# Kernel optimization log

Hardware: AMD Instinct MI355X
Metric: run time of the kernel (lower is better)

## Reference

```python
import jax, jax.numpy as jnp
import numpy as np

C0 = 32   # number of 0e (scalar) channels
C1 = 16   # number of 1o (vector) channels
NG = 1024 # num_graphs
N = 300000
F = C0 * (C0 + 1) // 2 + C1 * (C1 + 1) // 2  # 664 invariant outputs of TensorSquare->0e


def setup_inputs() -> dict:
    key = jax.random.key(0)
    k1, k2, k3 = jax.random.split(key, 3)
    node_ft = jax.random.normal(k1, (N, C0 + 3 * C1), dtype=jnp.float32)
    batch_index = jnp.sort(jax.random.randint(k2, (N,), 0, NG, dtype=jnp.int32))
    # o3.Linear-style init: normal / sqrt(fan_in)
    W = jax.random.normal(k3, (F, 1), dtype=jnp.float32) / np.float32(np.sqrt(F))
    return {"node_ft": node_ft, "batch_index": batch_index, "num_graphs": NG, "W": W}


def tensor_square_0e(node_ft):
    # Equivariant tensor square keeping only 0e (invariant) outputs:
    #  - symmetric products of scalar channels s_i * s_j (i<=j)
    #  - dot products of vector channels v_i . v_j (i<=j), component-normalized
    s = node_ft[:, :C0]                      # [N, C0]
    v = node_ft[:, C0:].reshape(-1, C1, 3)   # [N, C1, 3]
    i0, j0 = jnp.triu_indices(C0)
    i1, j1 = jnp.triu_indices(C1)
    ts_s = s[:, i0] * s[:, j0]                                  # [N, 528]
    vdot = jnp.einsum('nic,njc->nij', v, v) / jnp.float32(np.sqrt(3.0))
    ts_v = vdot[:, i1, j1]                                      # [N, 136]
    return jnp.concatenate([ts_s, ts_v], axis=1)                # [N, 664]


def reference(node_ft, batch_index, num_graphs, W):
    x = tensor_square_0e(node_ft)            # [N, F]
    x = jax.nn.selu(x)
    x = x @ W                                # [N, 1] attention logits (1x0e)
    ex = jnp.exp(x)                          # [N, 1]
    z = jax.ops.segment_sum(ex, batch_index, num_segments=num_graphs)  # [G, 1]
    attn = ex / z[batch_index]               # segment softmax weights [N, 1]
    out = jax.ops.segment_sum(node_ft * attn, batch_index, num_segments=num_graphs)
    return out                               # [G, C0 + 3*C1]
```

## Files before the change

kernel.cpp:

```cpp
#include <hip/hip_runtime.h>


typedef float f2 __attribute__((ext_vector_type(2)));

#define C0 32
#define C1 16
#define NODE_F 80
#define NG_CONST 1024
#define NPB 128
#define TPB 256
#define NCHUNK 6

#define SELU_SCALE 1.0507009873554804934193349852946
#define SELU_ALPHA 1.6732632423543772848170429916717
#define LOG2E      1.4426950408889634073599246810019

#define CS_SCALE 1.2011224087864498f
#define CV_SCALE 0.91271231102878545f

#define WS_S 0
#define WS_Z 81920
#define WS_W 82944

__device__ __forceinline__ int ks_idx(int i, int j) { return i * C0 - (i * (i - 1)) / 2 + (j - i); }
__device__ __forceinline__ int kv_idx(int i, int j) { return 528 + i * C1 - (i * (i - 1)) / 2 + (j - i); }

__global__ __launch_bounds__(256) void prep_kernel(
    const float* __restrict__ W, float* __restrict__ ws)
{
    const int t = blockIdx.x * blockDim.x + threadIdx.x;
    if (t < 82944) {
        ws[t] = 0.0f;
    } else {
        int u = t - 82944;
        if (u < 512) {
            int i = u >> 4, q = u & 15;
            int j0 = 2 * q, j1 = 2 * q + 1;
            ws[WS_W + 2 * u]     = (j0 >= i) ? W[ks_idx(i, j0)] : 0.0f;
            ws[WS_W + 2 * u + 1] = (j1 >= i) ? W[ks_idx(i, j1)] : 0.0f;
        } else if (u < 640) {
            int v = u - 512;
            int i = v >> 3, q = v & 7;
            int j0 = 2 * q, j1 = 2 * q + 1;
            ws[WS_W + 1024 + 2 * v]     = (j0 >= i) ? W[kv_idx(i, j0)] : 0.0f;
            ws[WS_W + 1024 + 2 * v + 1] = (j1 >= i) ? W[kv_idx(i, j1)] : 0.0f;
        }
    }
}

__global__ __launch_bounds__(TPB, 4) void main_kernel(
    const float* __restrict__ nf, const int* __restrict__ bi,
    const float* __restrict__ ws, float* __restrict__ S,
    float* __restrict__ z, int N)
{
    __shared__ __align__(16) float Wlds[1280];
    __shared__ float exl[NPB];
    __shared__ int   bil[NPB];

    const int tid  = threadIdx.x;
    const int base = blockIdx.x * NPB;
    const float4* g4 = (const float4*)nf;

    #pragma unroll
    for (int u = tid; u < 1280; u += TPB) Wlds[u] = ws[WS_W + u];

    if (tid < NPB) {
        int idx = base + tid;
        bil[tid] = bi[idx > N - 1 ? N - 1 : idx];
    }

    const int  ln    = tid >> 1;
    const int  p     = tid & 1;
    const int  n     = base + ln;
    const bool valid = (n < N);
    const int  nn    = valid ? n : (N - 1);
    __syncthreads();

    const float4* gp = g4 + (size_t)nn * 20;
    const f2* WsL = (const f2*)Wlds;
    const f2* WvL = (const f2*)(Wlds + 1024);

    f2 s2[C0 / 2];
    {
        float4 rs[8];
        #pragma unroll
        for (int q = 0; q < 8; ++q) rs[q] = gp[q];
        #pragma unroll
        for (int q = 0; q < 8; ++q) {
            s2[2 * q]     = f2{rs[q].x, rs[q].y} * CS_SCALE;
            s2[2 * q + 1] = f2{rs[q].z, rs[q].w} * CS_SCALE;
        }
    }
    #pragma unroll
    for (int q = 0; q < C0 / 2; ++q) asm volatile("" : "+v"(s2[q]));

    f2 accA[2], accB[2];
    accA[0] = (f2)0.f; accA[1] = (f2)0.f; accB[0] = (f2)0.f; accB[1] = (f2)0.f;

    #pragma unroll
    for (int k = 0; k < C0 / 2; ++k) {
        const int i = 2 * k + p;
        const float si = p ? s2[k].y : s2[k].x;
        const f2 si2 = f2{si, si};
        #pragma unroll
        for (int q = k; q < C0 / 2; ++q) {
            f2 f = si2 * s2[q];
            f2 pp = __builtin_elementwise_max(f, (f2)0.f);
            f2 m  = __builtin_elementwise_min(f, (f2)0.f);
            f2 e; e.x = __builtin_amdgcn_exp2f(m.x);
                  e.y = __builtin_amdgcn_exp2f(m.y);
            f2 w = WsL[i * 16 + q];
            accA[q & 1] = __builtin_elementwise_fma(w, pp, accA[q & 1]);
            accB[q & 1] = __builtin_elementwise_fma(w, e, accB[q & 1]);
        }
    }

    float4 rv[12];
    #pragma unroll
    for (int q = 0; q < 12; ++q) rv[q] = gp[8 + q];

    f2 vp[C1 / 2][3];
    {
        const float* rvf = (const float*)rv;
        #pragma unroll
        for (int q = 0; q < C1 / 2; ++q) {
            #pragma unroll
            for (int c = 0; c < 3; ++c)
                vp[q][c] = f2{rvf[6 * q + c], rvf[6 * q + 3 + c]} * CV_SCALE;
        }
    }

    #pragma unroll
    for (int k = 0; k < C1 / 2; ++k) {
        const int i = 2 * k + p;
        const float vi0 = p ? vp[k][0].y : vp[k][0].x;
        const float vi1 = p ? vp[k][1].y : vp[k][1].x;
        const float vi2 = p ? vp[k][2].y : vp[k][2].x;
        #pragma unroll
        for (int q = k; q < C1 / 2; ++q) {
            f2 f = vp[q][0] * f2{vi0, vi0};
            f = __builtin_elementwise_fma(vp[q][1], f2{vi1, vi1}, f);
            f = __builtin_elementwise_fma(vp[q][2], f2{vi2, vi2}, f);
            f2 pp = __builtin_elementwise_max(f, (f2)0.f);
            f2 m  = __builtin_elementwise_min(f, (f2)0.f);
            f2 e; e.x = __builtin_amdgcn_exp2f(m.x);
                  e.y = __builtin_amdgcn_exp2f(m.y);
            f2 w = WvL[i * 8 + q];
            accA[q & 1] = __builtin_elementwise_fma(w, pp, accA[q & 1]);
            accB[q & 1] = __builtin_elementwise_fma(w, e, accB[q & 1]);
        }
    }

    float A1 = accA[0].x + accA[0].y + accA[1].x + accA[1].y;
    float A2 = accB[0].x + accB[0].y + accB[1].x + accB[1].y;
    A1 += __shfl_xor(A1, 1);
    A2 += __shfl_xor(A2, 1);
    const float l2 = fmaf((float)SELU_SCALE, A1,
                          (float)(SELU_SCALE * SELU_ALPHA * LOG2E) * A2);
    if (p == 0) exl[ln] = valid ? __builtin_amdgcn_exp2f(l2) : 0.0f;
    __syncthreads();

    if (tid < NCHUNK * 20) {
        const int no = tid / 20;
        const int c4 = tid % 20;
        const int nb = (no * NPB) / NCHUNK;
        const int ne = ((no + 1) * NPB) / NCHUNK;
        int cg = bil[nb];
        float4 acc = make_float4(0.f, 0.f, 0.f, 0.f);
        float  zacc = 0.0f;

        for (int nl = nb; nl < ne; ++nl) {
            const int g2 = bil[nl];
            if (g2 != cg) {
                unsafeAtomicAdd(&S[cg * NODE_F + c4 * 4 + 0], acc.x);
                unsafeAtomicAdd(&S[cg * NODE_F + c4 * 4 + 1], acc.y);
                unsafeAtomicAdd(&S[cg * NODE_F + c4 * 4 + 2], acc.z);
                unsafeAtomicAdd(&S[cg * NODE_F + c4 * 4 + 3], acc.w);
                if (c4 == 0) unsafeAtomicAdd(&z[cg], zacc);
                acc = make_float4(0.f, 0.f, 0.f, 0.f); zacc = 0.0f; cg = g2;
            }
            int idx = base + nl; if (idx > N - 1) idx = N - 1;
            const float  w = exl[nl];
            const float4 v = g4[(size_t)idx * 20 + c4];
            acc.x = fmaf(v.x, w, acc.x); acc.y = fmaf(v.y, w, acc.y);
            acc.z = fmaf(v.z, w, acc.z); acc.w = fmaf(v.w, w, acc.w);
            zacc += w;
        }
        unsafeAtomicAdd(&S[cg * NODE_F + c4 * 4 + 0], acc.x);
        unsafeAtomicAdd(&S[cg * NODE_F + c4 * 4 + 1], acc.y);
        unsafeAtomicAdd(&S[cg * NODE_F + c4 * 4 + 2], acc.z);
        unsafeAtomicAdd(&S[cg * NODE_F + c4 * 4 + 3], acc.w);
        if (c4 == 0) unsafeAtomicAdd(&z[cg], zacc);
    }
}

__global__ __launch_bounds__(256) void divide_kernel(
    const float* __restrict__ S, const float* __restrict__ z,
    float* __restrict__ out)
{
    const int t = blockIdx.x * blockDim.x + threadIdx.x;
    if (t >= NG_CONST * NODE_F) return;
    const float zz = z[t / NODE_F];
    out[t] = (zz > 0.0f) ? (S[t] / zz) : 0.0f;
}

extern "C" void kernel_launch(void* const* d_in, const int* in_sizes, int n_in,
                              void* d_out, int out_size, void* d_ws, size_t ws_size,
                              hipStream_t stream) {
    const float* nf = (const float*)d_in[0];
    const int*   bi = (const int*)d_in[1];
    const float* W  = (const float*)d_in[3];
    float* out = (float*)d_out;

    const int N = in_sizes[0] / NODE_F;
    float* ws = (float*)d_ws;
    float* S  = ws + WS_S;
    float* z  = ws + WS_Z;

    hipLaunchKernelGGL(prep_kernel, dim3(332), dim3(256), 0, stream, W, ws);
    hipLaunchKernelGGL(main_kernel, dim3((N + NPB - 1) / NPB), dim3(TPB), 0, stream,
                       nf, bi, ws, S, z, N);
    hipLaunchKernelGGL(divide_kernel, dim3((NG_CONST * NODE_F + 255) / 256), dim3(256),
                       0, stream, S, z, out);
}
```

Measured before the change: 182.3 us.

## Split each node's tensor-square across four threads with padded LDS weight rows

Each node's pairwise product work is now split across four threads instead of two, and the block size doubles to 512 threads for the same 128 nodes. The weight table in LDS is repacked with padded row strides of 17 and 9, likely to avoid bank conflicts when four lanes read different rows. The aim is more parallelism per node and shorter per-thread dependency chains. The cost is an extra shuffle stage and redundant node loads in four threads, and the launch-bounds minimum-blocks hint of 4 at 512 threads may tighten the register budget.

After: 187.9 us. +3.1%, slower.

```diff
diff --git a/kernel.cpp b/kernel.cpp
--- a/kernel.cpp
+++ b/kernel.cpp
@@ -8,7 +8,7 @@
 #define NODE_F 80
 #define NG_CONST 1024
 #define NPB 128
-#define TPB 256
+#define TPB 512
 #define NCHUNK 6
 
 #define SELU_SCALE 1.0507009873554804934193349852946
@@ -33,17 +33,25 @@
         ws[t] = 0.0f;
     } else {
         int u = t - 82944;
-        if (u < 512) {
-            int i = u >> 4, q = u & 15;
-            int j0 = 2 * q, j1 = 2 * q + 1;
-            ws[WS_W + 2 * u]     = (j0 >= i) ? W[ks_idx(i, j0)] : 0.0f;
-            ws[WS_W + 2 * u + 1] = (j1 >= i) ? W[ks_idx(i, j1)] : 0.0f;
-        } else if (u < 640) {
-            int v = u - 512;
-            int i = v >> 3, q = v & 7;
-            int j0 = 2 * q, j1 = 2 * q + 1;
-            ws[WS_W + 1024 + 2 * v]     = (j0 >= i) ? W[kv_idx(i, j0)] : 0.0f;
-            ws[WS_W + 1024 + 2 * v + 1] = (j1 >= i) ? W[kv_idx(i, j1)] : 0.0f;
+        if (u < 1088) {
+            int fu = u >> 1, comp = u & 1;
+            int i = fu / 17, q = fu % 17;
+            float val = 0.0f;
+            if (q < 16) {
+                int j = 2 * q + comp;
+                val = (j >= i) ? W[ks_idx(i, j)] : 0.0f;
+            }
+            ws[WS_W + u] = val;
+        } else if (u < 1376) {
+            int v = u - 1088;
+            int fv = v >> 1, comp = v & 1;
+            int i = fv / 9, q = fv % 9;
+            float val = 0.0f;
+            if (q < 8) {
+                int j = 2 * q + comp;
+                val = (j >= i) ? W[kv_idx(i, j)] : 0.0f;
+            }
+            ws[WS_W + u] = val;
         }
     }
 }
@@ -53,7 +61,7 @@
     const float* __restrict__ ws, float* __restrict__ S,
     float* __restrict__ z, int N)
 {
-    __shared__ __align__(16) float Wlds[1280];
+    __shared__ __align__(16) float Wlds[1376];
     __shared__ float exl[NPB];
     __shared__ int   bil[NPB];
 
@@ -61,16 +69,17 @@
     const int base = blockIdx.x * NPB;
     const float4* g4 = (const float4*)nf;
 
-    #pragma unroll
-    for (int u = tid; u < 1280; u += TPB) Wlds[u] = ws[WS_W + u];
+    for (int u = tid; u < 1376; u += TPB) Wlds[u] = ws[WS_W + u];
 
     if (tid < NPB) {
         int idx = base + tid;
         bil[tid] = bi[idx > N - 1 ? N - 1 : idx];
     }
 
-    const int  ln    = tid >> 1;
-    const int  p     = tid & 1;
+    const int  ln    = tid >> 2;
+    const int  r     = tid & 3;
+    const bool rhi   = (r >= 2);
+    const bool rodd  = (r & 1) != 0;
     const int  n     = base + ln;
     const bool valid = (n < N);
     const int  nn    = valid ? n : (N - 1);
@@ -78,7 +87,7 @@
 
     const float4* gp = g4 + (size_t)nn * 20;
     const f2* WsL = (const f2*)Wlds;
-    const f2* WvL = (const f2*)(Wlds + 1024);
+    const f2* WvL = (const f2*)(Wlds + 1088);
 
     f2 s2[C0 / 2];
     {
@@ -98,18 +107,18 @@
     accA[0] = (f2)0.f; accA[1] = (f2)0.f; accB[0] = (f2)0.f; accB[1] = (f2)0.f;
 
     #pragma unroll
-    for (int k = 0; k < C0 / 2; ++k) {
-        const int i = 2 * k + p;
-        const float si = p ? s2[k].y : s2[k].x;
+    for (int k = 0; k < 8; ++k) {
+        const f2 sp = rhi ? s2[2 * k + 1] : s2[2 * k];
+        const float si = rodd ? sp.y : sp.x;
         const f2 si2 = f2{si, si};
         #pragma unroll
-        for (int q = k; q < C0 / 2; ++q) {
+        for (int q = 2 * k; q < 16; ++q) {
             f2 f = si2 * s2[q];
             f2 pp = __builtin_elementwise_max(f, (f2)0.f);
             f2 m  = __builtin_elementwise_min(f, (f2)0.f);
             f2 e; e.x = __builtin_amdgcn_exp2f(m.x);
                   e.y = __builtin_amdgcn_exp2f(m.y);
-            f2 w = WsL[i * 16 + q];
+            f2 w = WsL[(4 * k + r) * 17 + q];
             accA[q & 1] = __builtin_elementwise_fma(w, pp, accA[q & 1]);
             accB[q & 1] = __builtin_elementwise_fma(w, e, accB[q & 1]);
         }
@@ -131,13 +140,15 @@
     }
 
     #pragma unroll
-    for (int k = 0; k < C1 / 2; ++k) {
-        const int i = 2 * k + p;
-        const float vi0 = p ? vp[k][0].y : vp[k][0].x;
-        const float vi1 = p ? vp[k][1].y : vp[k][1].x;
-        const float vi2 = p ? vp[k][2].y : vp[k][2].x;
-        #pragma unroll
-        for (int q = k; q < C1 / 2; ++q) {
+    for (int k = 0; k < 4; ++k) {
+        const f2 a0 = rhi ? vp[2 * k + 1][0] : vp[2 * k][0];
+        const f2 a1 = rhi ? vp[2 * k + 1][1] : vp[2 * k][1];
+        const f2 a2 = rhi ? vp[2 * k + 1][2] : vp[2 * k][2];
+        const float vi0 = rodd ? a0.y : a0.x;
+        const float vi1 = rodd ? a1.y : a1.x;
+        const float vi2 = rodd ? a2.y : a2.x;
+        #pragma unroll
+        for (int q = 2 * k; q < 8; ++q) {
             f2 f = vp[q][0] * f2{vi0, vi0};
             f = __builtin_elementwise_fma(vp[q][1], f2{vi1, vi1}, f);
             f = __builtin_elementwise_fma(vp[q][2], f2{vi2, vi2}, f);
@@ -145,7 +156,7 @@
             f2 m  = __builtin_elementwise_min(f, (f2)0.f);
             f2 e; e.x = __builtin_amdgcn_exp2f(m.x);
                   e.y = __builtin_amdgcn_exp2f(m.y);
-            f2 w = WvL[i * 8 + q];
+            f2 w = WvL[(4 * k + r) * 9 + q];
             accA[q & 1] = __builtin_elementwise_fma(w, pp, accA[q & 1]);
             accB[q & 1] = __builtin_elementwise_fma(w, e, accB[q & 1]);
         }
@@ -153,11 +164,11 @@
 
     float A1 = accA[0].x + accA[0].y + accA[1].x + accA[1].y;
     float A2 = accB[0].x + accB[0].y + accB[1].x + accB[1].y;
-    A1 += __shfl_xor(A1, 1);
-    A2 += __shfl_xor(A2, 1);
+    A1 += __shfl_xor(A1, 1);  A1 += __shfl_xor(A1, 2);
+    A2 += __shfl_xor(A2, 1);  A2 += __shfl_xor(A2, 2);
     const float l2 = fmaf((float)SELU_SCALE, A1,
                           (float)(SELU_SCALE * SELU_ALPHA * LOG2E) * A2);
-    if (p == 0) exl[ln] = valid ? __builtin_amdgcn_exp2f(l2) : 0.0f;
+    if (r == 0) exl[ln] = valid ? __builtin_amdgcn_exp2f(l2) : 0.0f;
     __syncthreads();
 
     if (tid < NCHUNK * 20) {
```
